# Performance work log

Hardware: AMD Instinct MI355X
Metric: run time of the kernel (lower is better)

The kernel has to match this reference:

```python
import jax, jax.numpy as jnp
import numpy as np

B = 65536
V = 7          # vertices
OPD = 48       # op_embedding_dim
ND = 48        # node_embedding_dim
HID = 96       # hid_dim
GD = 128       # gcn out dim
NOPS = 32      # op embedding table size
NONE_OP = 3
MLP_DIMS = [200, 200, 200]


def _flow(y, adj, op_emb, W, attW, attb, bias):
    # DenseGraphFlow: support = y @ W; out = sigmoid(op_emb @ attW + attb) * (adj @ support) + support + bias
    support = jnp.einsum('bvi,io->bvo', y, W)
    gate = jax.nn.sigmoid(jnp.einsum('bve,eo->bvo', op_emb, attW) + attb)
    return gate * jnp.einsum('bvw,bwo->bvo', adj, support) + support + bias


def _forward(x_adj_1, zcp, op_emb_table, input_op_emb, output_op_emb,
             input_node_emb, other_node_emb, xh_W, xh_b,
             gcn0_W, gcn0_attW, gcn0_attb, gcn0_bias,
             gcn_W, gcn_attW, gcn_attb, gcn_bias,
             mlp0_W, mlp0_b, mlp1_W, mlp1_b, mlp2_W, mlp2_b, mlp3_W, mlp3_b,
             x_ops_1):
    b = x_ops_1.shape[0]
    adjs = jnp.transpose(x_adj_1, (0, 2, 1))              # archs use arch.T
    op_inds = x_ops_1[:, 1:-1]                            # [B, V-2]
    mid_op = op_emb_table[op_inds]                        # [B, V-2, OPD]
    op_embs = jnp.concatenate([
        jnp.broadcast_to(input_op_emb[None], (b, 1, OPD)),
        mid_op,
        jnp.broadcast_to(output_op_emb[None], (b, 1, OPD)),
    ], axis=1)                                            # [B, V, OPD]
    node_embs = jnp.concatenate([
        jnp.broadcast_to(input_node_emb[None], (b, 1, ND)),
        jnp.broadcast_to(other_node_emb[None], (b, V - 1, ND)),
    ], axis=1)                                            # [B, V, ND]
    x = jnp.einsum('bvn,nh->bvh', node_embs, xh_W) + xh_b  # [B, V, HID]

    # GCN stack: layer 0 (HID->GD), then 4 layers (GD->GD); relu except last
    y = _flow(x, adjs, op_embs, gcn0_W, gcn0_attW, gcn0_attb, gcn0_bias)
    y = jax.nn.relu(y)
    n_rest = gcn_W.shape[0]
    for i in range(n_rest):
        y = _flow(y, adjs, op_embs, gcn_W[i], gcn_attW[i], gcn_attb[i], gcn_bias[i])
        if i != n_rest - 1:
            y = jax.nn.relu(y)

    # final process: drop input node, mask none-ops, mean over nodes
    y = y[:, 1:, :]                                       # [B, V-1, GD]
    mask = (op_inds != NONE_OP).astype(jnp.float32)[:, :, None]
    y = jnp.concatenate([y[:, :-1, :] * mask, y[:, -1:, :]], axis=1)
    y = jnp.mean(y, axis=1)                               # [B, GD]

    # MLP head (dropout inactive / eval)
    y = jax.nn.relu(y @ mlp0_W + mlp0_b)
    y = jax.nn.relu(y @ mlp1_W + mlp1_b)
    y = jax.nn.relu(y @ mlp2_W + mlp2_b)
    y = y @ mlp3_W + mlp3_b                               # [B, 1]
    return y


def setup_inputs() -> dict:
    key = jax.random.key(0)
    ks = iter(jax.random.split(key, 40))
    u = lambda shape, s: jax.random.uniform(next(ks), shape, jnp.float32, -s, s)
    inp = {}
    inp['x_ops_1'] = jax.random.randint(next(ks), (B, V), 0, NOPS, dtype=jnp.int64)
    inp['x_adj_1'] = jax.random.uniform(next(ks), (B, V, V), jnp.float32)
    inp['zcp'] = jax.random.normal(next(ks), (B, 13), jnp.float32)
    inp['op_emb_table'] = jax.random.normal(next(ks), (NOPS, OPD), jnp.float32)
    inp['input_op_emb'] = jnp.zeros((1, OPD), jnp.float32)
    inp['output_op_emb'] = jax.random.normal(next(ks), (1, OPD), jnp.float32)
    inp['input_node_emb'] = jax.random.normal(next(ks), (1, ND), jnp.float32)
    inp['other_node_emb'] = jnp.zeros((1, ND), jnp.float32)
    inp['xh_W'] = u((ND, HID), 1.0 / np.sqrt(ND))
    inp['xh_b'] = u((HID,), 1.0 / np.sqrt(ND))
    s = 1.0 / np.sqrt(GD)
    inp['gcn0_W'] = u((HID, GD), s)
    inp['gcn0_attW'] = u((OPD, GD), 1.0 / np.sqrt(OPD))
    inp['gcn0_attb'] = u((GD,), 1.0 / np.sqrt(OPD))
    inp['gcn0_bias'] = u((GD,), s)
    inp['gcn_W'] = u((4, GD, GD), s)
    inp['gcn_attW'] = u((4, OPD, GD), 1.0 / np.sqrt(OPD))
    inp['gcn_attb'] = u((4, GD), 1.0 / np.sqrt(OPD))
    inp['gcn_bias'] = u((4, GD), s)
    d = GD
    for i, h in enumerate(MLP_DIMS):
        inp[f'mlp{i}_W'] = u((d, h), 1.0 / np.sqrt(d))
        inp[f'mlp{i}_b'] = u((h,), 1.0 / np.sqrt(d))
        d = h
    inp['mlp3_W'] = u((d, 1), 1.0 / np.sqrt(d))
    inp['mlp3_b'] = u((1,), 1.0 / np.sqrt(d))
    return inp


def reference(x_ops_1, x_adj_1, zcp, op_emb_table, input_op_emb, output_op_emb,
              input_node_emb, other_node_emb, xh_W, xh_b,
              gcn0_W, gcn0_attW, gcn0_attb, gcn0_bias,
              gcn_W, gcn_attW, gcn_attb, gcn_bias,
              mlp0_W, mlp0_b, mlp1_W, mlp1_b, mlp2_W, mlp2_b, mlp3_W, mlp3_b):
    return _forward(x_adj_1, zcp, op_emb_table, input_op_emb, output_op_emb,
                    input_node_emb, other_node_emb, xh_W, xh_b,
                    gcn0_W, gcn0_attW, gcn0_attb, gcn0_bias,
                    gcn_W, gcn_attW, gcn_attb, gcn_bias,
                    mlp0_W, mlp0_b, mlp1_W, mlp1_b, mlp2_W, mlp2_b, mlp3_W, mlp3_b,
                    x_ops_1)
```

## Files before the change

### kernel.cpp

```cpp
#include <hip/hip_runtime.h>
#include <math.h>

#define V 7
#define OPD 48
#define HID 96
#define GD 128
#define NGATE 34
#define NONE_OP 3
#define NB 16

typedef unsigned short u16;
typedef unsigned int u32;
typedef _Float16 f16;
typedef __attribute__((ext_vector_type(8))) _Float16 f16x8;
typedef __attribute__((ext_vector_type(4))) float f32x4;

#define RSCALE 2048.0f
#define RINV   (1.0f/2048.0f)

#define WS_GATES   0u
#define WS_SUP0    87040u
#define WS_GWH     90624u
#define WS_GWL     221696u
#define WS_W0H     352768u
#define WS_W0L     406016u
#define WS_W1H     459264u
#define WS_W1L     552448u
#define WS_W2H     645632u
#define WS_W2L     738816u

#define S_YH   0u
#define S_YL   32768u
#define S_SUPT 0u
#define S_ADJ  65536u
#define S_SUP0 69120u
#define S_BIAS 73216u
#define S_GI   75776u
#define S_TOTAL 76288u
#define S_ZH   0u
#define S_ZL   4096u
#define S_A1H  8192u
#define S_A1L  16384u
#define S_A2H  24576u
#define S_A2L  32768u

__device__ __forceinline__ u32 sw256(u32 row, u32 kb) { return row * 256u + (kb ^ ((row & 7u) << 4)); }
__device__ __forceinline__ u32 sw512(u32 row, u32 kb) { return row * 512u + (kb ^ ((row & 7u) << 4)); }
__device__ __forceinline__ u32 ssw(u32 col, u32 rb) { return col * 512u + (rb ^ (((col ^ (col >> 3)) & 7u) << 4)); }

#define MFMA(a, b, c) __builtin_amdgcn_mfma_f32_16x16x32_f16(a, b, c, 0, 0, 0)

__global__ __launch_bounds__(256) void precompute_kernel(
    const float* __restrict__ op_tbl, const float* __restrict__ in_op,
    const float* __restrict__ out_op, const float* __restrict__ in_node,
    const float* __restrict__ other_node, const float* __restrict__ xh_W,
    const float* __restrict__ xh_b, const float* __restrict__ g0W,
    const float* __restrict__ g0attW, const float* __restrict__ g0attb,
    const float* __restrict__ gattW, const float* __restrict__ gattb,
    const float* __restrict__ gW, const float* __restrict__ m0W,
    const float* __restrict__ m1W, const float* __restrict__ m2W,
    char* __restrict__ ws)
{
  const int blk = blockIdx.x, tid = threadIdx.x;
  float* gates = (float*)(ws + WS_GATES);
  float* sup0 = (float*)(ws + WS_SUP0);
  if (blk < 85) {
    const int row = blk * 2 + (tid >> 7);
    const int c = tid & 127;
    const int l = row / NGATE, e = row % NGATE;
    const float* emb = (e < 32) ? (op_tbl + e * OPD) : (e == 32 ? in_op : out_op);
    const float* aW = (l == 0) ? g0attW : (gattW + (size_t)(l - 1) * OPD * GD);
    const float* ab = (l == 0) ? g0attb : (gattb + (l - 1) * GD);
    float acc = ab[c];
    for (int j = 0; j < OPD; j++) acc += emb[j] * aW[j * GD + c];
    gates[(size_t)row * GD + c] = 1.0f / (1.0f + expf(-acc));
  } else if (blk == 85) {
    __shared__ float x[V * HID];
    for (int i = tid; i < V * HID; i += 256) {
      const int v = i / HID, h = i % HID;
      const float* emb = (v == 0) ? in_node : other_node;
      float acc = xh_b[h];
      for (int j = 0; j < 48; j++) acc += emb[j] * xh_W[j * HID + h];
      x[i] = acc;
    }
    __syncthreads();
    for (int i = tid; i < V * GD; i += 256) {
      const int v = i / GD, c = i % GD;
      float acc = 0.f;
      for (int h = 0; h < HID; h++) acc += x[v * HID + h] * g0W[h * GD + c];
      sup0[i] = acc;
    }
  } else {
    for (int idx = (blk - 86) * 256 + tid; idx < 185344; idx += 128 * 256) {
      float w; f16 *ph, *pl;
      if (idx < 65536) {
        const int l = idx >> 14, rem = idx & 16383;
        const int n = rem >> 7, k = rem & 127;
        w = gW[(size_t)l * 16384 + k * 128 + n];
        ph = (f16*)(ws + WS_GWH) + idx; pl = (f16*)(ws + WS_GWL) + idx;
      } else if (idx < 92160) {
        const int j = idx - 65536, n = j >> 7, k = j & 127;
        w = (n < 200) ? m0W[(size_t)k * 200 + n] : 0.f;
        ph = (f16*)(ws + WS_W0H) + j; pl = (f16*)(ws + WS_W0L) + j;
      } else if (idx < 138752) {
        const int j = idx - 92160, n = j / 224, k = j % 224;
        w = (n < 200 && k < 200) ? m1W[(size_t)k * 200 + n] : 0.f;
        ph = (f16*)(ws + WS_W1H) + j; pl = (f16*)(ws + WS_W1L) + j;
      } else {
        const int j = idx - 138752, n = j / 224, k = j % 224;
        w = (n < 200 && k < 200) ? m2W[(size_t)k * 200 + n] : 0.f;
        ph = (f16*)(ws + WS_W2H) + j; pl = (f16*)(ws + WS_W2L) + j;
      }
      const f16 h = (f16)w;
      *ph = h;
      *pl = (f16)((w - (float)h) * RSCALE);
    }
  }
}

__global__ __launch_bounds__(256, 2) void gin_main_kernel(
    const int* __restrict__ x_ops, const float* __restrict__ x_adj,
    const char* __restrict__ ws,
    const float* __restrict__ g0_bias, const float* __restrict__ gcn_bias,
    const float* __restrict__ m0b, const float* __restrict__ m1b,
    const float* __restrict__ m2b, const float* __restrict__ m3W,
    const float* __restrict__ m3b, float* __restrict__ out)
{
  extern __shared__ char smem[];
  const int tid = threadIdx.x;
  const int bbase = blockIdx.x * NB;
  const float* gates_ws = (const float*)(ws + WS_GATES);
  const float* sup0_ws = (const float*)(ws + WS_SUP0);
  const f16* GWH = (const f16*)(ws + WS_GWH);
  const f16* GWL = (const f16*)(ws + WS_GWL);
  const f16* W0H = (const f16*)(ws + WS_W0H);
  const f16* W0L = (const f16*)(ws + WS_W0L);
  const f16* W1H = (const f16*)(ws + WS_W1H);
  const f16* W1L = (const f16*)(ws + WS_W1L);
  const f16* W2H = (const f16*)(ws + WS_W2H);
  const f16* W2L = (const f16*)(ws + WS_W2L);

  for (int i = tid; i < 16 * 56; i += 256) {
    const int s = i / 56, r = i % 56, v = r >> 3, w = r & 7;
    ((float*)(smem + S_ADJ))[i] = (w < 7) ? x_adj[(size_t)(bbase + s) * 49 + w * 7 + v] : 0.f;
  }
  if (tid < 128) {
    const int s = tid >> 3, v = tid & 7;
    const int g = (v == 0) ? 32 : (v == 6) ? 33 : (v == 7) ? 0
                : x_ops[(size_t)(bbase + s) * 7 + v];
    ((int*)(smem + S_GI))[tid] = g;
  }
  for (int i = tid; i < 1024; i += 256) {
    const int col = i >> 3, v = i & 7;
    ((float*)(smem + S_SUP0))[i] = (v < 7) ? sup0_ws[v * 128 + col] : 0.f;
  }
  for (int i = tid; i < 640; i += 256) {
    const int l = i >> 7, c = i & 127;
    ((float*)(smem + S_BIAS))[i] = (l == 0) ? g0_bias[c] : gcn_bias[(l - 1) * 128 + c];
  }
  __syncthreads();

  const int lane = tid & 63, wave = tid >> 6;
  const int lrow = lane & 15, lq = lane >> 4;
  const int ms = tid >> 4;
  const int colbase = (tid & 15) * 8;

  for (int l = 0; l < 5; l++) {
    if (l > 0) {
      const f16* wh = GWH + (l - 1) * 16384;
      const f16* wl = GWL + (l - 1) * 16384;
      f32x4 acc0[8][2], acc1[8][2];
#pragma unroll
      for (int t = 0; t < 8; t++)
#pragma unroll
        for (int nt = 0; nt < 2; nt++) {
          acc0[t][nt] = (f32x4){0.f, 0.f, 0.f, 0.f};
          acc1[t][nt] = (f32x4){0.f, 0.f, 0.f, 0.f};
        }
#pragma unroll
      for (int ks = 0; ks < 4; ks++) {
        f16x8 bh[2], bl[2];
#pragma unroll
        for (int nt = 0; nt < 2; nt++) {
          const int eo = (wave * 32 + nt * 16 + lrow) * 128 + ks * 32 + lq * 8;
          bh[nt] = *(const f16x8*)(wh + eo);
          bl[nt] = *(const f16x8*)(wl + eo);
        }
#pragma unroll
        for (int t = 0; t < 8; t++) {
          const u32 off = sw256((u32)(t * 16 + lrow), (u32)(ks * 64 + lq * 16));
          const f16x8 ah = *(const f16x8*)(smem + S_YH + off);
          const f16x8 al = *(const f16x8*)(smem + S_YL + off);
#pragma unroll
          for (int nt = 0; nt < 2; nt++) {
            acc0[t][nt] = MFMA(ah, bh[nt], acc0[t][nt]);
            acc1[t][nt] = MFMA(ah, bl[nt], acc1[t][nt]);
            acc1[t][nt] = MFMA(al, bh[nt], acc1[t][nt]);
          }
        }
      }
      __syncthreads();
#pragma unroll
      for (int t = 0; t < 8; t++)
#pragma unroll
        for (int nt = 0; nt < 2; nt++) {
          const u32 col = (u32)(wave * 32 + nt * 16 + lrow);
          f32x4 vv;
#pragma unroll
          for (int r = 0; r < 4; r++) vv[r] = acc0[t][nt][r] + acc1[t][nt][r] * RINV;
          *(f32x4*)(smem + S_SUPT + ssw(col, (u32)(t * 64 + lq * 16))) = vv;
        }
      __syncthreads();
    }

    f32x4 sa[8], sb[8];
    if (l == 0) {
#pragma unroll
      for (int c = 0; c < 8; c++) {
        const u32 o = (u32)(colbase + c) * 32u;
        sa[c] = *(const f32x4*)(smem + S_SUP0 + o);
        sb[c] = *(const f32x4*)(smem + S_SUP0 + o + 16);
      }
    } else {
#pragma unroll
      for (int c = 0; c < 8; c++) {
        const u32 col = (u32)(colbase + c);
        sa[c] = *(const f32x4*)(smem + S_SUPT + ssw(col, (u32)(ms * 32)));
        sb[c] = *(const f32x4*)(smem + S_SUPT + ssw(col, (u32)(ms * 32 + 16)));
      }
      __syncthreads();
    }

    {
      const f32x4 bb0 = *(const f32x4*)(smem + S_BIAS + (l * 128 + colbase) * 4);
      const f32x4 bb1 = *(const f32x4*)(smem + S_BIAS + (l * 128 + colbase) * 4 + 16);
      const int* giv = (const int*)(smem + S_GI) + ms * 8;
      float zacc[8];
#pragma unroll
      for (int c = 0; c < 8; c++) zacc[c] = 0.f;
#pragma unroll
      for (int v = 0; v < 7; v++) {
        const f32x4 a0 = *(const f32x4*)(smem + S_ADJ + (ms * 56 + v * 8) * 4);
        const f32x4 a1 = *(const f32x4*)(smem + S_ADJ + (ms * 56 + v * 8) * 4 + 16);
        const int gidx = giv[v];
        const f32x4* gp = (const f32x4*)(gates_ws + ((size_t)l * NGATE + gidx) * 128 + colbase);
        const f32x4 g0 = gp[0], g1 = gp[1];
        float y[8];
#pragma unroll
        for (int c = 0; c < 8; c++) {
          const float t = a0[0] * sa[c][0] + a0[1] * sa[c][1] + a0[2] * sa[c][2] + a0[3] * sa[c][3]
                        + a1[0] * sb[c][0] + a1[1] * sb[c][1] + a1[2] * sb[c][2];
          const float sv = (v < 4) ? sa[c][v] : sb[c][v - 4];
          const float gg = (c < 4) ? g0[c] : g1[c - 4];
          const float bv = (c < 4) ? bb0[c] : bb1[c - 4];
          y[c] = gg * t + sv + bv;
        }
        if (l < 4) {
          union { f16x8 v8; f16 e[8]; } ph, pl;
#pragma unroll
          for (int c = 0; c < 8; c++) {
            const float r = fmaxf(y[c], 0.f);
            const f16 h = (f16)r;
            ph.e[c] = h;
            pl.e[c] = (f16)((r - (float)h) * RSCALE);
          }
          const u32 yo = sw256((u32)(ms * 8 + v), (u32)(colbase * 2));
          *(f16x8*)(smem + S_YH + yo) = ph.v8;
          *(f16x8*)(smem + S_YL + yo) = pl.v8;
        } else {
          if ((v == 6) || (v >= 1 && gidx != NONE_OP))
#pragma unroll
            for (int c = 0; c < 8; c++) zacc[c] += y[c];
        }
      }
      if (l == 4) {
        union { f16x8 v8; f16 e[8]; } ph, pl;
#pragma unroll
        for (int c = 0; c < 8; c++) {
          const float z = zacc[c] * (1.f / 6.f);
          const f16 h = (f16)z;
          ph.e[c] = h;
          pl.e[c] = (f16)((z - (float)h) * RSCALE);
        }
        const u32 zo = sw256((u32)ms, (u32)(colbase * 2));
        *(f16x8*)(smem + S_ZH + zo) = ph.v8;
        *(f16x8*)(smem + S_ZL + zo) = pl.v8;
        for (int i = tid; i < 8192; i += 256) ((u32*)(smem + S_A1H))[i] = 0u;
      }
    }
    __syncthreads();
  }

  {
    f32x4 macc0[4], macc1[4];
#pragma unroll
    for (int i = 0; i < 4; i++) { macc0[i] = (f32x4){0.f,0.f,0.f,0.f}; macc1[i] = (f32x4){0.f,0.f,0.f,0.f}; }
#pragma unroll
    for (int ks = 0; ks < 4; ks++) {
      const u32 off = sw256((u32)lrow, (u32)(ks * 64 + lq * 16));
      const f16x8 zh = *(const f16x8*)(smem + S_ZH + off);
      const f16x8 zl = *(const f16x8*)(smem + S_ZL + off);
#pragma unroll
      for (int i = 0; i < 4; i++) {
        const int nt = wave + i * 4;
        if (nt < 13) {
          const int eo = (nt * 16 + lrow) * 128 + ks * 32 + lq * 8;
          const f16x8 wh8 = *(const f16x8*)(W0H + eo);
          const f16x8 wl8 = *(const f16x8*)(W0L + eo);
          macc0[i] = MFMA(zh, wh8, macc0[i]);
          macc1[i] = MFMA(zh, wl8, macc1[i]);
          macc1[i] = MFMA(zl, wh8, macc1[i]);
        }
      }
    }
#pragma unroll
    for (int i = 0; i < 4; i++) {
      const int nt = wave + i * 4;
      if (nt < 13) {
        const int col = nt * 16 + lrow;
        const float b = (col < 200) ? m0b[col] : 0.f;
#pragma unroll
        for (int r = 0; r < 4; r++) {
          const float a = fmaxf(macc0[i][r] + macc1[i][r] * RINV + b, 0.f);
          const f16 h = (f16)a;
          const u32 off = sw512((u32)(lq * 4 + r), (u32)(2 * col));
          *(f16*)(smem + S_A1H + off) = h;
          *(f16*)(smem + S_A1L + off) = (f16)((a - (float)h) * RSCALE);
        }
      }
    }
  }
  __syncthreads();
  {
    f32x4 macc0[4], macc1[4];
#pragma unroll
    for (int i = 0; i < 4; i++) { macc0[i] = (f32x4){0.f,0.f,0.f,0.f}; macc1[i] = (f32x4){0.f,0.f,0.f,0.f}; }
#pragma unroll
    for (int ks = 0; ks < 7; ks++) {
      const u32 off = sw512((u32)lrow, (u32)(ks * 64 + lq * 16));
      const f16x8 ah = *(const f16x8*)(smem + S_A1H + off);
      const f16x8 al = *(const f16x8*)(smem + S_A1L + off);
#pragma unroll
      for (int i = 0; i < 4; i++) {
        const int nt = wave + i * 4;
        if (nt < 13) {
          const int eo = (nt * 16 + lrow) * 224 + ks * 32 + lq * 8;
          const f16x8 wh8 = *(const f16x8*)(W1H + eo);
          const f16x8 wl8 = *(const f16x8*)(W1L + eo);
          macc0[i] = MFMA(ah, wh8, macc0[i]);
          macc1[i] = MFMA(ah, wl8, macc1[i]);
          macc1[i] = MFMA(al, wh8, macc1[i]);
        }
      }
    }
#pragma unroll
    for (int i = 0; i < 4; i++) {
      const int nt = wave + i * 4;
      if (nt < 13) {
        const int col = nt * 16 + lrow;
        const float b = (col < 200) ? m1b[col] : 0.f;
#pragma unroll
        for (int r = 0; r < 4; r++) {
          const float a = fmaxf(macc0[i][r] + macc1[i][r] * RINV + b, 0.f);
          const f16 h = (f16)a;
          const u32 off = sw512((u32)(lq * 4 + r), (u32)(2 * col));
          *(f16*)(smem + S_A2H + off) = h;
          *(f16*)(smem + S_A2L + off) = (f16)((a - (float)h) * RSCALE);
        }
      }
    }
  }
  __syncthreads();
  {
    f32x4 macc0[4], macc1[4];
#pragma unroll
    for (int i = 0; i < 4; i++) { macc0[i] = (f32x4){0.f,0.f,0.f,0.f}; macc1[i] = (f32x4){0.f,0.f,0.f,0.f}; }
#pragma unroll
    for (int ks = 0; ks < 7; ks++) {
      const u32 off = sw512((u32)lrow, (u32)(ks * 64 + lq * 16));
      const f16x8 ah = *(const f16x8*)(smem + S_A2H + off);
      const f16x8 al = *(const f16x8*)(smem + S_A2L + off);
#pragma unroll
      for (int i = 0; i < 4; i++) {
        const int nt = wave + i * 4;
        if (nt < 13) {
          const int eo = (nt * 16 + lrow) * 224 + ks * 32 + lq * 8;
          const f16x8 wh8 = *(const f16x8*)(W2H + eo);
          const f16x8 wl8 = *(const f16x8*)(W2L + eo);
          macc0[i] = MFMA(ah, wh8, macc0[i]);
          macc1[i] = MFMA(ah, wl8, macc1[i]);
          macc1[i] = MFMA(al, wh8, macc1[i]);
        }
      }
    }
#pragma unroll
    for (int i = 0; i < 4; i++) {
      const int nt = wave + i * 4;
      if (nt < 13) {
        const int col = nt * 16 + lrow;
        const float b = (col < 200) ? m2b[col] : 0.f;
#pragma unroll
        for (int r = 0; r < 4; r++) {
          const float a = fmaxf(macc0[i][r] + macc1[i][r] * RINV + b, 0.f);
          const f16 h = (f16)a;
          const u32 off = sw512((u32)(lq * 4 + r), (u32)(2 * col));
          *(f16*)(smem + S_A1H + off) = h;
          *(f16*)(smem + S_A1L + off) = (f16)((a - (float)h) * RSCALE);
        }
      }
    }
  }
  __syncthreads();
  {
    const int kl = tid & 15;
    float p = 0.f;
    for (int k = kl; k < 200; k += 16) {
      const u32 off = sw512((u32)ms, (u32)(2 * k));
      const float a = (float)(*(const f16*)(smem + S_A1H + off))
                    + (float)(*(const f16*)(smem + S_A1L + off)) * RINV;
      p += a * m3W[k];
    }
#pragma unroll
    for (int d = 8; d > 0; d >>= 1) p += __shfl_down(p, d, 16);
    if (kl == 0) out[bbase + ms] = p + m3b[0];
  }
}

extern "C" void kernel_launch(void* const* d_in, const int* in_sizes, int n_in,
                              void* d_out, int out_size, void* d_ws, size_t ws_size,
                              hipStream_t stream) {
  const int*   x_ops    = (const int*)  d_in[0];
  const float* x_adj    = (const float*)d_in[1];
  const float* op_tbl   = (const float*)d_in[3];
  const float* in_op    = (const float*)d_in[4];
  const float* out_op   = (const float*)d_in[5];
  const float* in_node  = (const float*)d_in[6];
  const float* oth_node = (const float*)d_in[7];
  const float* xh_W     = (const float*)d_in[8];
  const float* xh_b     = (const float*)d_in[9];
  const float* g0W      = (const float*)d_in[10];
  const float* g0attW   = (const float*)d_in[11];
  const float* g0attb   = (const float*)d_in[12];
  const float* g0bias   = (const float*)d_in[13];
  const float* gW       = (const float*)d_in[14];
  const float* gattW    = (const float*)d_in[15];
  const float* gattb    = (const float*)d_in[16];
  const float* gbias    = (const float*)d_in[17];
  const float* m0W = (const float*)d_in[18], *m0b = (const float*)d_in[19];
  const float* m1W = (const float*)d_in[20], *m1b = (const float*)d_in[21];
  const float* m2W = (const float*)d_in[22], *m2b = (const float*)d_in[23];
  const float* m3W = (const float*)d_in[24], *m3b = (const float*)d_in[25];
  float* out = (float*)d_out;
  char* ws = (char*)d_ws;
  (void)ws_size; (void)n_in; (void)out_size;

  const int B = in_sizes[0] / V;
  const int nblk = B / NB;

  hipFuncSetAttribute((const void*)gin_main_kernel,
                      hipFuncAttributeMaxDynamicSharedMemorySize, (int)S_TOTAL);

  hipLaunchKernelGGL(precompute_kernel, dim3(214), dim3(256), 0, stream,
                     op_tbl, in_op, out_op, in_node, oth_node, xh_W, xh_b,
                     g0W, g0attW, g0attb, gattW, gattb, gW, m0W, m1W, m2W, ws);
  hipLaunchKernelGGL(gin_main_kernel, dim3(nblk), dim3(256), (int)S_TOTAL, stream,
                     x_ops, x_adj, (const char*)ws, g0bias, gbias,
                     m0b, m1b, m2b, m3W, m3b, out);
}
```

Baseline: 504.2 us.

## Halve per-block batch, shrink LDS, drop split-precision low parts in MLP

Cuts the samples per block from 16 to 8 and moves the layer-0 support and bias reads from shared memory to global memory. This roughly halves shared-memory use, so four blocks per CU can be resident instead of two. It also drops the low-order f16 half of the activations feeding the last two MLP layers and the final dot product, which removes one MFMA per step and some shared-memory traffic. In exchange, the weight tiles are reused across fewer rows per block, and the MLP tail loses precision.

```diff
diff --git a/kernel.cpp b/kernel.cpp
--- a/kernel.cpp
+++ b/kernel.cpp
@@ -7,11 +7,12 @@
 #define GD 128
 #define NGATE 34
 #define NONE_OP 3
-#define NB 16
+#define NB 8
 
 typedef unsigned short u16;
 typedef unsigned int u32;
 typedef _Float16 f16;
+typedef __attribute__((ext_vector_type(4))) _Float16 f16x4;
 typedef __attribute__((ext_vector_type(8))) _Float16 f16x8;
 typedef __attribute__((ext_vector_type(4))) float f32x4;
 
@@ -19,34 +20,31 @@
 #define RINV   (1.0f/2048.0f)
 
 #define WS_GATES   0u
-#define WS_SUP0    87040u
-#define WS_GWH     90624u
-#define WS_GWL     221696u
-#define WS_W0H     352768u
-#define WS_W0L     406016u
-#define WS_W1H     459264u
-#define WS_W1L     552448u
-#define WS_W2H     645632u
-#define WS_W2L     738816u
+#define WS_SUP0T   87040u
+#define WS_GWH     91136u
+#define WS_GWL     222208u
+#define WS_W0H     353280u
+#define WS_W0L     406528u
+#define WS_W1H     459776u
+#define WS_W1L     552960u
+#define WS_W2H     646144u
+#define WS_W2L     739328u
 
 #define S_YH   0u
-#define S_YL   32768u
+#define S_YL   16384u
 #define S_SUPT 0u
-#define S_ADJ  65536u
-#define S_SUP0 69120u
-#define S_BIAS 73216u
-#define S_GI   75776u
-#define S_TOTAL 76288u
+#define S_ADJ  32768u
+#define S_GI   34560u
+#define S_TOTAL 34816u
 #define S_ZH   0u
 #define S_ZL   4096u
 #define S_A1H  8192u
 #define S_A1L  16384u
 #define S_A2H  24576u
-#define S_A2L  32768u
 
 __device__ __forceinline__ u32 sw256(u32 row, u32 kb) { return row * 256u + (kb ^ ((row & 7u) << 4)); }
 __device__ __forceinline__ u32 sw512(u32 row, u32 kb) { return row * 512u + (kb ^ ((row & 7u) << 4)); }
-__device__ __forceinline__ u32 ssw(u32 col, u32 rb) { return col * 512u + (rb ^ (((col ^ (col >> 3)) & 7u) << 4)); }
+__device__ __forceinline__ u32 ssw(u32 col, u32 rb) { return col * 256u + (rb ^ (((col ^ (col >> 3)) & 7u) << 4)); }
 
 #define MFMA(a, b, c) __builtin_amdgcn_mfma_f32_16x16x32_f16(a, b, c, 0, 0, 0)
 
@@ -63,7 +61,7 @@
 {
   const int blk = blockIdx.x, tid = threadIdx.x;
   float* gates = (float*)(ws + WS_GATES);
-  float* sup0 = (float*)(ws + WS_SUP0);
+  float* sup0T = (float*)(ws + WS_SUP0T);
   if (blk < 85) {
     const int row = blk * 2 + (tid >> 7);
     const int c = tid & 127;
@@ -88,8 +86,9 @@
       const int v = i / GD, c = i % GD;
       float acc = 0.f;
       for (int h = 0; h < HID; h++) acc += x[v * HID + h] * g0W[h * GD + c];
-      sup0[i] = acc;
-    }
+      sup0T[c * 8 + v] = acc;
+    }
+    for (int i = tid; i < GD; i += 256) sup0T[i * 8 + 7] = 0.f;
   } else {
     for (int idx = (blk - 86) * 256 + tid; idx < 185344; idx += 128 * 256) {
       float w; f16 *ph, *pl;
@@ -118,7 +117,7 @@
   }
 }
 
-__global__ __launch_bounds__(256, 2) void gin_main_kernel(
+__global__ __launch_bounds__(256, 4) void gin_main_kernel(
     const int* __restrict__ x_ops, const float* __restrict__ x_adj,
     const char* __restrict__ ws,
     const float* __restrict__ g0_bias, const float* __restrict__ gcn_bias,
@@ -130,7 +129,7 @@
   const int tid = threadIdx.x;
   const int bbase = blockIdx.x * NB;
   const float* gates_ws = (const float*)(ws + WS_GATES);
-  const float* sup0_ws = (const float*)(ws + WS_SUP0);
+  const float* sup0T = (const float*)(ws + WS_SUP0T);
   const f16* GWH = (const f16*)(ws + WS_GWH);
   const f16* GWL = (const f16*)(ws + WS_GWL);
   const f16* W0H = (const f16*)(ws + WS_W0H);
@@ -140,38 +139,30 @@
   const f16* W2H = (const f16*)(ws + WS_W2H);
   const f16* W2L = (const f16*)(ws + WS_W2L);
 
-  for (int i = tid; i < 16 * 56; i += 256) {
+  for (int i = tid; i < NB * 56; i += 256) {
     const int s = i / 56, r = i % 56, v = r >> 3, w = r & 7;
     ((float*)(smem + S_ADJ))[i] = (w < 7) ? x_adj[(size_t)(bbase + s) * 49 + w * 7 + v] : 0.f;
   }
-  if (tid < 128) {
+  if (tid < 64) {
     const int s = tid >> 3, v = tid & 7;
     const int g = (v == 0) ? 32 : (v == 6) ? 33 : (v == 7) ? 0
                 : x_ops[(size_t)(bbase + s) * 7 + v];
     ((int*)(smem + S_GI))[tid] = g;
   }
-  for (int i = tid; i < 1024; i += 256) {
-    const int col = i >> 3, v = i & 7;
-    ((float*)(smem + S_SUP0))[i] = (v < 7) ? sup0_ws[v * 128 + col] : 0.f;
-  }
-  for (int i = tid; i < 640; i += 256) {
-    const int l = i >> 7, c = i & 127;
-    ((float*)(smem + S_BIAS))[i] = (l == 0) ? g0_bias[c] : gcn_bias[(l - 1) * 128 + c];
-  }
   __syncthreads();
 
   const int lane = tid & 63, wave = tid >> 6;
   const int lrow = lane & 15, lq = lane >> 4;
-  const int ms = tid >> 4;
-  const int colbase = (tid & 15) * 8;
+  const int ms = tid >> 5;
+  const int colbase = (tid & 31) * 4;
 
   for (int l = 0; l < 5; l++) {
     if (l > 0) {
       const f16* wh = GWH + (l - 1) * 16384;
       const f16* wl = GWL + (l - 1) * 16384;
-      f32x4 acc0[8][2], acc1[8][2];
-#pragma unroll
-      for (int t = 0; t < 8; t++)
+      f32x4 acc0[4][2], acc1[4][2];
+#pragma unroll
+      for (int t = 0; t < 4; t++)
 #pragma unroll
         for (int nt = 0; nt < 2; nt++) {
           acc0[t][nt] = (f32x4){0.f, 0.f, 0.f, 0.f};
@@ -187,7 +178,7 @@
           bl[nt] = *(const f16x8*)(wl + eo);
         }
 #pragma unroll
-        for (int t = 0; t < 8; t++) {
+        for (int t = 0; t < 4; t++) {
           const u32 off = sw256((u32)(t * 16 + lrow), (u32)(ks * 64 + lq * 16));
           const f16x8 ah = *(const f16x8*)(smem + S_YH + off);
           const f16x8 al = *(const f16x8*)(smem + S_YL + off);
@@ -201,7 +192,7 @@
       }
       __syncthreads();
 #pragma unroll
-      for (int t = 0; t < 8; t++)
+      for (int t = 0; t < 4; t++)
 #pragma unroll
         for (int nt = 0; nt < 2; nt++) {
           const u32 col = (u32)(wave * 32 + nt * 16 + lrow);
@@ -213,17 +204,17 @@
       __syncthreads();
     }
 
-    f32x4 sa[8], sb[8];
+    f32x4 sa[4], sb[4];
     if (l == 0) {
 #pragma unroll
-      for (int c = 0; c < 8; c++) {
-        const u32 o = (u32)(colbase + c) * 32u;
-        sa[c] = *(const f32x4*)(smem + S_SUP0 + o);
-        sb[c] = *(const f32x4*)(smem + S_SUP0 + o + 16);
+      for (int c = 0; c < 4; c++) {
+        const float* p = sup0T + (size_t)(colbase + c) * 8;
+        sa[c] = *(const f32x4*)p;
+        sb[c] = *(const f32x4*)(p + 4);
       }
     } else {
 #pragma unroll
-      for (int c = 0; c < 8; c++) {
+      for (int c = 0; c < 4; c++) {
         const u32 col = (u32)(colbase + c);
         sa[c] = *(const f32x4*)(smem + S_SUPT + ssw(col, (u32)(ms * 32)));
         sb[c] = *(const f32x4*)(smem + S_SUPT + ssw(col, (u32)(ms * 32 + 16)));
@@ -232,60 +223,62 @@
     }
 
     {
-      const f32x4 bb0 = *(const f32x4*)(smem + S_BIAS + (l * 128 + colbase) * 4);
-      const f32x4 bb1 = *(const f32x4*)(smem + S_BIAS + (l * 128 + colbase) * 4 + 16);
+      const float* bias_l = (l == 0) ? g0_bias : gcn_bias + (l - 1) * GD;
+      const f32x4 bb = *(const f32x4*)(bias_l + colbase);
       const int* giv = (const int*)(smem + S_GI) + ms * 8;
-      float zacc[8];
-#pragma unroll
-      for (int c = 0; c < 8; c++) zacc[c] = 0.f;
+      float zacc[4];
+#pragma unroll
+      for (int c = 0; c < 4; c++) zacc[c] = 0.f;
 #pragma unroll
       for (int v = 0; v < 7; v++) {
         const f32x4 a0 = *(const f32x4*)(smem + S_ADJ + (ms * 56 + v * 8) * 4);
         const f32x4 a1 = *(const f32x4*)(smem + S_ADJ + (ms * 56 + v * 8) * 4 + 16);
         const int gidx = giv[v];
-        const f32x4* gp = (const f32x4*)(gates_ws + ((size_t)l * NGATE + gidx) * 128 + colbase);
-        const f32x4 g0 = gp[0], g1 = gp[1];
-        float y[8];
-#pragma unroll
-        for (int c = 0; c < 8; c++) {
+        const f32x4 gg = *(const f32x4*)(gates_ws + ((size_t)l * NGATE + gidx) * GD + colbase);
+        float y[4];
+#pragma unroll
+        for (int c = 0; c < 4; c++) {
           const float t = a0[0] * sa[c][0] + a0[1] * sa[c][1] + a0[2] * sa[c][2] + a0[3] * sa[c][3]
                         + a1[0] * sb[c][0] + a1[1] * sb[c][1] + a1[2] * sb[c][2];
           const float sv = (v < 4) ? sa[c][v] : sb[c][v - 4];
-          const float gg = (c < 4) ? g0[c] : g1[c - 4];
-          const float bv = (c < 4) ? bb0[c] : bb1[c - 4];
-          y[c] = gg * t + sv + bv;
+          y[c] = gg[c] * t + sv + bb[c];
         }
         if (l < 4) {
-          union { f16x8 v8; f16 e[8]; } ph, pl;
-#pragma unroll
-          for (int c = 0; c < 8; c++) {
+          union { f16x4 v4; f16 e[4]; } ph, pl;
+#pragma unroll
+          for (int c = 0; c < 4; c++) {
             const float r = fmaxf(y[c], 0.f);
             const f16 h = (f16)r;
             ph.e[c] = h;
             pl.e[c] = (f16)((r - (float)h) * RSCALE);
           }
           const u32 yo = sw256((u32)(ms * 8 + v), (u32)(colbase * 2));
-          *(f16x8*)(smem + S_YH + yo) = ph.v8;
-          *(f16x8*)(smem + S_YL + yo) = pl.v8;
+          *(f16x4*)(smem + S_YH + yo) = ph.v4;
+          *(f16x4*)(smem + S_YL + yo) = pl.v4;
         } else {
           if ((v == 6) || (v >= 1 && gidx != NONE_OP))
 #pragma unroll
-            for (int c = 0; c < 8; c++) zacc[c] += y[c];
+            for (int c = 0; c < 4; c++) zacc[c] += y[c];
         }
       }
       if (l == 4) {
-        union { f16x8 v8; f16 e[8]; } ph, pl;
-#pragma unroll
-        for (int c = 0; c < 8; c++) {
+        union { f16x4 v4; f16 e[4]; } ph, pl;
+#pragma unroll
+        for (int c = 0; c < 4; c++) {
           const float z = zacc[c] * (1.f / 6.f);
           const f16 h = (f16)z;
           ph.e[c] = h;
           pl.e[c] = (f16)((z - (float)h) * RSCALE);
         }
         const u32 zo = sw256((u32)ms, (u32)(colbase * 2));
-        *(f16x8*)(smem + S_ZH + zo) = ph.v8;
-        *(f16x8*)(smem + S_ZL + zo) = pl.v8;
-        for (int i = tid; i < 8192; i += 256) ((u32*)(smem + S_A1H))[i] = 0u;
+        *(f16x4*)(smem + S_ZH + zo) = ph.v4;
+        *(f16x4*)(smem + S_ZL + zo) = pl.v4;
+        for (int i = tid; i < 512; i += 256) {
+          ((u32*)(smem + S_ZH + 2048u))[i] = 0u;
+          ((u32*)(smem + S_ZL + 2048u))[i] = 0u;
+        }
+        for (int i = tid; i < 6144; i += 256)
+          ((u32*)(smem + S_A1H))[i] = 0u;
       }
     }
     __syncthreads();
@@ -362,10 +355,8 @@
 #pragma unroll
         for (int r = 0; r < 4; r++) {
           const float a = fmaxf(macc0[i][r] + macc1[i][r] * RINV + b, 0.f);
-          const f16 h = (f16)a;
           const u32 off = sw512((u32)(lq * 4 + r), (u32)(2 * col));
-          *(f16*)(smem + S_A2H + off) = h;
-          *(f16*)(smem + S_A2L + off) = (f16)((a - (float)h) * RSCALE);
+          *(f16*)(smem + S_A2H + off) = (f16)a;
         }
       }
     }
@@ -379,7 +370,6 @@
     for (int ks = 0; ks < 7; ks++) {
       const u32 off = sw512((u32)lrow, (u32)(ks * 64 + lq * 16));
       const f16x8 ah = *(const f16x8*)(smem + S_A2H + off);
-      const f16x8 al = *(const f16x8*)(smem + S_A2L + off);
 #pragma unroll
       for (int i = 0; i < 4; i++) {
         const int nt = wave + i * 4;
@@ -389,10 +379,10 @@
           const f16x8 wl8 = *(const f16x8*)(W2L + eo);
           macc0[i] = MFMA(ah, wh8, macc0[i]);
           macc1[i] = MFMA(ah, wl8, macc1[i]);
-          macc1[i] = MFMA(al, wh8, macc1[i]);
-        }
-      }
-    }
+        }
+      }
+    }
+    __syncthreads();
 #pragma unroll
     for (int i = 0; i < 4; i++) {
       const int nt = wave + i * 4;
@@ -402,26 +392,22 @@
 #pragma unroll
         for (int r = 0; r < 4; r++) {
           const float a = fmaxf(macc0[i][r] + macc1[i][r] * RINV + b, 0.f);
-          const f16 h = (f16)a;
           const u32 off = sw512((u32)(lq * 4 + r), (u32)(2 * col));
-          *(f16*)(smem + S_A1H + off) = h;
-          *(f16*)(smem + S_A1L + off) = (f16)((a - (float)h) * RSCALE);
+          *(f16*)(smem + S_A1H + off) = (f16)a;
         }
       }
     }
   }
   __syncthreads();
   {
-    const int kl = tid & 15;
+    const int kl = tid & 31;
     float p = 0.f;
-    for (int k = kl; k < 200; k += 16) {
+    for (int k = kl; k < 200; k += 32) {
       const u32 off = sw512((u32)ms, (u32)(2 * k));
-      const float a = (float)(*(const f16*)(smem + S_A1H + off))
-                    + (float)(*(const f16*)(smem + S_A1L + off)) * RINV;
-      p += a * m3W[k];
-    }
-#pragma unroll
-    for (int d = 8; d > 0; d >>= 1) p += __shfl_down(p, d, 16);
+      p += (float)(*(const f16*)(smem + S_A1H + off)) * m3W[k];
+    }
+#pragma unroll
+    for (int d = 16; d > 0; d >>= 1) p += __shfl_down(p, d, 32);
     if (kl == 0) out[bbase + ms] = p + m3b[0];
   }
 }
```

New measurement: 748.3 us. 1.48x slower.
